# Kernel tuning notes

Hardware: AMD Instinct MI355X
Metric: run time of the kernel (lower is better)

## Reference

```python
import jax, jax.numpy as jnp
import numpy as np

NUM_CLASSES = 9
BASE_SMOOTHING = 0.1
UPWARD_BIAS = 0.2
BATCH = 4_000_000


def setup_inputs() -> dict:
    key = jax.random.key(0)
    k1, k2 = jax.random.split(key)
    logits = jax.random.normal(k1, (BATCH, NUM_CLASSES), dtype=jnp.float32)
    targets = jax.random.randint(k2, (BATCH,), 0, NUM_CLASSES, dtype=jnp.int32)
    return {"logits": logits, "targets": targets}


def _smooth_labels(targets, num_classes):
    # Closed form of the per-sample Python loop in the torch module:
    #   label[t] = 1 - bs - ub  (set, overwriting the base)
    #   label[k] = bs/C + ub * 0.5**(k - t)   for k > t (geometric halving,
    #              including the last class which keeps remaining*0.5)
    #   label[k] = bs/C                        for k < t
    # followed by row normalization.
    base = BASE_SMOOTHING / num_classes
    main = 1.0 - BASE_SMOOTHING - UPWARD_BIAS
    j = jnp.arange(num_classes)  # [C]
    d = j[None, :] - targets[:, None]  # [B, C], class index minus target
    upward = jnp.where(d > 0, UPWARD_BIAS * jnp.exp2(-d.astype(jnp.float32)), 0.0)
    labels = jnp.where(d == 0, main, base + upward)  # [B, C]
    return labels / labels.sum(axis=-1, keepdims=True)


def reference(logits, targets):
    smooth = _smooth_labels(targets, logits.shape[-1])  # [B, C]
    log_probs = jax.nn.log_softmax(logits, axis=-1)      # [B, C]
    loss = -(smooth * log_probs).sum(axis=-1)            # [B]
    return loss.mean()
```

## Files before the change

### kernel.cpp

```cpp
#include <hip/hip_runtime.h>
#include <math.h>

#define NUM_C 9
constexpr float W_BASE = 0.1f / 9.0f;
constexpr float W_MAIN = 0.7f;

constexpr int THREADS = 256;
constexpr int GRID = 512;
constexpr int CHUNK_ROWS = 1024;
constexpr int VECS_PER_CHUNK = CHUNK_ROWS * NUM_C / 4;
constexpr int VECS_PER_WAVE  = VECS_PER_CHUNK / 4;
constexpr int CALLS_PER_WAVE = VECS_PER_WAVE / 64;
constexpr int TVECS_PER_CHUNK = CHUNK_ROWS / 4;

__device__ __forceinline__ void async_copy16(const void* g, void* l) {
    __builtin_amdgcn_global_load_lds(
        (const __attribute__((address_space(1))) void*)g,
        (__attribute__((address_space(3))) void*)l,
        16 , 0 , 0 );
}

__device__ __forceinline__ void stage_chunk(
    const float4* __restrict__ logv, const int4* __restrict__ tgtv,
    float4* lbuf, int4* tbuf, int chunk, int wave, int lane)
{
    const float4* src = logv + (long long)chunk * VECS_PER_CHUNK + wave * VECS_PER_WAVE;
    float4* dst = lbuf + wave * VECS_PER_WAVE;
#pragma unroll
    for (int i = 0; i < CALLS_PER_WAVE; i++)
        async_copy16(src + i * 64 + lane, dst + i * 64);
    async_copy16(tgtv + (long long)chunk * TVECS_PER_CHUNK + wave * 64 + lane,
                 tbuf + wave * 64);
}

__device__ __forceinline__ float rows4_loss(const float* x, const int4& t4) {
    const int tg[4] = {t4.x, t4.y, t4.z, t4.w};
    float acc = 0.0f;
#pragma unroll
    for (int k = 0; k < 4; k++) {
        const float* xr = x + k * NUM_C;
        const int t = tg[k];

        float m = xr[0];
#pragma unroll
        for (int j = 1; j < NUM_C; j++) m = fmaxf(m, xr[j]);

        float sum = 0.0f, xt = 0.0f;
#pragma unroll
        for (int j = 0; j < NUM_C; j++) {
            sum += xr[j];
            xt = (t == j) ? xr[j] : xt;
        }

        float g = 0.0f, gt = 0.0f;
#pragma unroll
        for (int j = NUM_C - 1; j >= 1; j--) {
            g = 0.5f * (xr[j] + g);
            gt = (t == j - 1) ? g : gt;
        }

        float es = 0.0f;
#pragma unroll
        for (int j = 0; j < NUM_C; j++) es += __expf(xr[j] - m);
        const float lse = m + __logf(es);

        const float S = 0.98888889f - 0.2f * ldexpf(1.0f, t - 8);
        const float weighted = W_BASE * sum + (W_MAIN - W_BASE) * xt + 0.2f * gt;
        acc += lse - weighted * __builtin_amdgcn_rcpf(S);
    }
    return acc;
}

__global__ __launch_bounds__(THREADS, 2) void ccel_main(
    const float* __restrict__ logits,
    const int* __restrict__ targets,
    float* __restrict__ partials,
    int nRows)
{
    __shared__ float4 lds4[2][VECS_PER_CHUNK];
    __shared__ int4   tlds[2][TVECS_PER_CHUNK];

    const int tid  = threadIdx.x;
    const int wave = tid >> 6;
    const int lane = tid & 63;
    const int bid  = blockIdx.x;

    const float4* logv = (const float4*)logits;
    const int4*   tgtv = (const int4*)targets;

    const int nFull = nRows / CHUNK_ROWS;

    float acc = 0.0f;

    if (bid < nFull)
        stage_chunk(logv, tgtv, &lds4[0][0], &tlds[0][0], bid, wave, lane);

    int cur = 0;
    for (int c = bid; c < nFull; c += GRID) {
        const int cn = c + GRID;
        asm volatile("s_waitcnt lgkmcnt(0)" ::: "memory");
        if (cn < nFull) {
            stage_chunk(logv, tgtv, &lds4[cur ^ 1][0], &tlds[cur ^ 1][0],
                        cn, wave, lane);
            asm volatile("s_waitcnt vmcnt(10)" ::: "memory");
        } else {
            asm volatile("s_waitcnt vmcnt(0)" ::: "memory");
        }
        __builtin_amdgcn_sched_barrier(0);

        float x[36];
        float4* xv = (float4*)x;
#pragma unroll
        for (int i = 0; i < 9; i++) xv[i] = lds4[cur][tid * 9 + i];
        const int4 t4 = tlds[cur][tid];

        acc += rows4_loss(x, t4);

        __builtin_amdgcn_sched_barrier(0);
        cur ^= 1;
    }

    const int tailRows = nRows - nFull * CHUNK_ROWS;
    if (tailRows > 0 && bid == (nFull % GRID)) {
        const long long rowBase = (long long)nFull * CHUNK_ROWS;
        const int myRow = tid * 4;
        if (myRow + 4 <= tailRows) {
            float x[36];
            float4* xv = (float4*)x;
            const float4* gp = logv + (rowBase * NUM_C) / 4 + tid * 9;
#pragma unroll
            for (int i = 0; i < 9; i++) xv[i] = gp[i];
            const int4 t4 = tgtv[rowBase / 4 + tid];
            acc += rows4_loss(x, t4);
        }
    }

#pragma unroll
    for (int off = 32; off > 0; off >>= 1)
        acc += __shfl_down(acc, off, 64);

    __syncthreads();
    float* wsum = (float*)&tlds[0][0];
    if (lane == 0) wsum[wave] = acc;
    __syncthreads();
    if (tid == 0) {
        float bsum = 0.0f;
#pragma unroll
        for (int w = 0; w < THREADS / 64; w++) bsum += wsum[w];
        partials[bid] = bsum;
    }
}

__global__ __launch_bounds__(1024) void ccel_finish(
    const float* __restrict__ partials,
    int n,
    float* __restrict__ out,
    float invBatch)
{
    double acc = 0.0;
    for (int i = threadIdx.x; i < n; i += 1024)
        acc += (double)partials[i];

#pragma unroll
    for (int off = 32; off > 0; off >>= 1)
        acc += __shfl_down(acc, off, 64);

    __shared__ double wsum[16];
    if ((threadIdx.x & 63) == 0) wsum[threadIdx.x >> 6] = acc;
    __syncthreads();
    if (threadIdx.x == 0) {
        double total = 0.0;
#pragma unroll
        for (int w = 0; w < 16; w++) total += wsum[w];
        out[0] = (float)(total * (double)invBatch);
    }
}

extern "C" void kernel_launch(void* const* d_in, const int* in_sizes, int n_in,
                              void* d_out, int out_size, void* d_ws, size_t ws_size,
                              hipStream_t stream) {
    const float* logits = (const float*)d_in[0];
    const int* targets = (const int*)d_in[1];
    const int nRows = in_sizes[1];

    float* partials = (float*)d_ws;

    ccel_main<<<GRID, THREADS, 0, stream>>>(logits, targets, partials, nRows);
    ccel_finish<<<1, 1024, 0, stream>>>(partials, GRID, (float*)d_out,
                                        1.0f / (float)nRows);
}
```

Measured before the change: 217.0 us.

## Halve chunk size, double grid and occupancy, process two rows per thread

Chunks shrink from 1024 to 512 rows and the grid grows from 512 to 1024 blocks. Launch bounds now ask for 4 blocks per CU instead of 2, and each thread handles 2 rows loaded as float2 instead of 4 rows as float4. Async LDS staging is redistributed unevenly across the four waves, and the hand-written waitcnt and sched_barrier sequence is replaced by a __syncthreads at the top of each iteration. The aim is more memory-level parallelism and latency hiding in this bandwidth-limited reduction, at the cost of more blocks and partials and a full-block barrier per chunk.

```diff
diff --git a/kernel.cpp b/kernel.cpp
--- a/kernel.cpp
+++ b/kernel.cpp
@@ -6,11 +6,9 @@
 constexpr float W_MAIN = 0.7f;
 
 constexpr int THREADS = 256;
-constexpr int GRID = 512;
-constexpr int CHUNK_ROWS = 1024;
+constexpr int GRID = 1024;
+constexpr int CHUNK_ROWS = 512;
 constexpr int VECS_PER_CHUNK = CHUNK_ROWS * NUM_C / 4;
-constexpr int VECS_PER_WAVE  = VECS_PER_CHUNK / 4;
-constexpr int CALLS_PER_WAVE = VECS_PER_WAVE / 64;
 constexpr int TVECS_PER_CHUNK = CHUNK_ROWS / 4;
 
 __device__ __forceinline__ void async_copy16(const void* g, void* l) {
@@ -22,22 +20,29 @@
 
 __device__ __forceinline__ void stage_chunk(
     const float4* __restrict__ logv, const int4* __restrict__ tgtv,
-    float4* lbuf, int4* tbuf, int chunk, int wave, int lane)
+    float4* lbuf, int4* tbuf, long long chunk, int wave, int lane)
 {
-    const float4* src = logv + (long long)chunk * VECS_PER_CHUNK + wave * VECS_PER_WAVE;
-    float4* dst = lbuf + wave * VECS_PER_WAVE;
+    const float4* src = logv + chunk * VECS_PER_CHUNK;
+    if (wave < 2) {
+        const int base = wave * 320;
 #pragma unroll
-    for (int i = 0; i < CALLS_PER_WAVE; i++)
-        async_copy16(src + i * 64 + lane, dst + i * 64);
-    async_copy16(tgtv + (long long)chunk * TVECS_PER_CHUNK + wave * 64 + lane,
-                 tbuf + wave * 64);
+        for (int i = 0; i < 5; i++)
+            async_copy16(src + base + i * 64 + lane, lbuf + base + i * 64);
+    } else {
+        const int base = 640 + (wave - 2) * 256;
+#pragma unroll
+        for (int i = 0; i < 4; i++)
+            async_copy16(src + base + i * 64 + lane, lbuf + base + i * 64);
+        const int tb = (wave - 2) * 64;
+        async_copy16(tgtv + chunk * TVECS_PER_CHUNK + tb + lane, tbuf + tb);
+    }
 }
 
-__device__ __forceinline__ float rows4_loss(const float* x, const int4& t4) {
-    const int tg[4] = {t4.x, t4.y, t4.z, t4.w};
+__device__ __forceinline__ float rows2_loss(const float* x, int t0, int t1) {
+    const int tg[2] = {t0, t1};
     float acc = 0.0f;
 #pragma unroll
-    for (int k = 0; k < 4; k++) {
+    for (int k = 0; k < 2; k++) {
         const float* xr = x + k * NUM_C;
         const int t = tg[k];
 
@@ -71,7 +76,7 @@
     return acc;
 }
 
-__global__ __launch_bounds__(THREADS, 2) void ccel_main(
+__global__ __launch_bounds__(THREADS, 4) void ccel_main(
     const float* __restrict__ logits,
     const int* __restrict__ targets,
     float* __restrict__ partials,
@@ -91,47 +96,42 @@
     const int nFull = nRows / CHUNK_ROWS;
 
     float acc = 0.0f;
+    int cur = 0;
 
     if (bid < nFull)
         stage_chunk(logv, tgtv, &lds4[0][0], &tlds[0][0], bid, wave, lane);
 
-    int cur = 0;
     for (int c = bid; c < nFull; c += GRID) {
+        __syncthreads();
         const int cn = c + GRID;
-        asm volatile("s_waitcnt lgkmcnt(0)" ::: "memory");
-        if (cn < nFull) {
+        if (cn < nFull)
             stage_chunk(logv, tgtv, &lds4[cur ^ 1][0], &tlds[cur ^ 1][0],
                         cn, wave, lane);
-            asm volatile("s_waitcnt vmcnt(10)" ::: "memory");
-        } else {
-            asm volatile("s_waitcnt vmcnt(0)" ::: "memory");
-        }
-        __builtin_amdgcn_sched_barrier(0);
 
-        float x[36];
-        float4* xv = (float4*)x;
+        const float2* lb2 = (const float2*)&lds4[cur][0];
+        const int2*   tb2 = (const int2*)&tlds[cur][0];
+        float x[18];
+        float2* xv = (float2*)x;
 #pragma unroll
-        for (int i = 0; i < 9; i++) xv[i] = lds4[cur][tid * 9 + i];
-        const int4 t4 = tlds[cur][tid];
+        for (int i = 0; i < 9; i++) xv[i] = lb2[tid * 9 + i];
+        const int2 t2 = tb2[tid];
 
-        acc += rows4_loss(x, t4);
-
-        __builtin_amdgcn_sched_barrier(0);
+        acc += rows2_loss(x, t2.x, t2.y);
         cur ^= 1;
     }
 
     const int tailRows = nRows - nFull * CHUNK_ROWS;
     if (tailRows > 0 && bid == (nFull % GRID)) {
         const long long rowBase = (long long)nFull * CHUNK_ROWS;
-        const int myRow = tid * 4;
-        if (myRow + 4 <= tailRows) {
-            float x[36];
-            float4* xv = (float4*)x;
-            const float4* gp = logv + (rowBase * NUM_C) / 4 + tid * 9;
+        const int myRow = tid * 2;
+        if (myRow + 2 <= tailRows) {
+            float x[18];
+            float2* xv = (float2*)x;
+            const float2* gp = (const float2*)(logits + rowBase * NUM_C) + tid * 9;
 #pragma unroll
             for (int i = 0; i < 9; i++) xv[i] = gp[i];
-            const int4 t4 = tgtv[rowBase / 4 + tid];
-            acc += rows4_loss(x, t4);
+            const int2 t2 = ((const int2*)targets)[rowBase / 2 + tid];
+            acc += rows2_loss(x, t2.x, t2.y);
         }
     }
 
```

New measurement: 215.2 us. No clear change (-0.8%).
